# Kernel tuning notes

Hardware: AMD Instinct MI355X
Metric: run time of the kernel (lower is better)

## Reference

```python
import jax, jax.numpy as jnp
import numpy as np
from jax import lax

T, B, E = 512, 128, 128  # timesteps, batch, embedding_size
S = 2 * T                # stack capacity: 2 pushes per step


def setup_inputs() -> dict:
    key = jax.random.key(0)
    k1, k2, k3, k4, k5 = jax.random.split(key, 5)
    return {
        "v1": jax.random.normal(k1, (T, B, E), dtype=jnp.float32),
        "v2": jax.random.normal(k2, (T, B, E), dtype=jnp.float32),
        "d1": jax.random.uniform(k3, (T, B, 1), dtype=jnp.float32),
        "d2": jax.random.uniform(k4, (T, B, 1), dtype=jnp.float32),
        "u": jax.random.uniform(k5, (T, B, 1), dtype=jnp.float32),
    }


def _step(carry, xs):
    strengths, values = carry  # [B,S], [B,S,E]; slots 0..2(t+1)-1 valid after push
    v1t, v2t, d1t, d2t, ut, t = xs  # v*: [B,E]; d*,u: [B,1]; t: scalar int
    # --- push: append two entries at the top (slots 2t, 2t+1) ---
    values = lax.dynamic_update_slice(
        values, jnp.stack([v1t, v2t], axis=1), (0, 2 * t, 0))
    strengths = lax.dynamic_update_slice(
        strengths, jnp.concatenate([d1t, d2t], axis=1), (0, 2 * t))
    # exclusive reverse cumsum = strength used above each slot (top-down order)
    rev_incl = jnp.flip(jnp.cumsum(jnp.flip(strengths, 1), axis=1), 1)  # [B,S]
    used = rev_incl - strengths  # [B,S]
    # --- read: faithful to torch.max(u - strength_used) reducing over batch ---
    m = jnp.max(ut - used, axis=0)            # [S] scalar-over-batch per slot
    w = jnp.minimum(strengths, m[None, :])    # [B,S]; invalid slots hit v=0
    summary = jnp.einsum('bs,bse->be', w, values)  # [B,E]
    # --- pop: s -= min(s, relu(u - used)) using pre-pop strengths ---
    pop_amt = jnp.minimum(strengths, jnp.maximum(0.0, ut - used))
    strengths = strengths - pop_amt
    return (strengths, values), summary


def reference(v1, v2, d1, d2, u):
    init = (jnp.zeros((B, S), v1.dtype), jnp.zeros((B, S, E), v1.dtype))
    ts = jnp.arange(T, dtype=jnp.int32)
    _, out = lax.scan(_step, init, (v1, v2, d1, d2, u, ts))
    return out  # [T,B,E]: read content at each timestep
```

## Files before the change

kernel.cpp:

```cpp
#include <hip/hip_runtime.h>
#include <cstdint>
#include <cstddef>

#define TT 512
#define BB 128
#define EE 128
#define SS 1024
#define NEG_INF (-1e30f)

typedef _Float16 half8 __attribute__((ext_vector_type(8)));
typedef float floatx4 __attribute__((ext_vector_type(4)));

__device__ __forceinline__ unsigned int pkh(float x, float y) {
    _Float16 hx = (_Float16)x, hy = (_Float16)y;
    unsigned short bx, by;
    __builtin_memcpy(&bx, &hx, 2); __builtin_memcpy(&by, &hy, 2);
    return (unsigned int)bx | ((unsigned int)by << 16);
}

__global__ __launch_bounds__(64) void prefixF(
    const float* __restrict__ d1, const float* __restrict__ d2,
    const float* __restrict__ u,
    float* __restrict__ F, float* __restrict__ Bv,
    float* __restrict__ d2T, float* __restrict__ FT,
    float* __restrict__ BvT, float* __restrict__ CST,
    float* __restrict__ CMT, float* __restrict__ HT)
{
    const int b = blockIdx.x;
    const int lane = threadIdx.x;
    const int t0 = lane * 8;

    float l1[8], l2[8], g[8];
#pragma unroll
    for (int j = 0; j < 8; ++j) {
        const int t = t0 + j;
        l1[j] = d1[t * BB + b];
        l2[j] = d2[t * BB + b];
        g[j] = u[t * BB + b] - l1[j] - l2[j];
    }
    float p[8], s = 0.f;
#pragma unroll
    for (int j = 0; j < 8; ++j) { s += g[j]; p[j] = s; }

    float v = s;
#pragma unroll
    for (int off = 1; off < 64; off <<= 1) {
        float o = __shfl_up(v, off);
        if (lane >= off) v += o;
    }
    const float excl = v - s;

    float Fv[8];
#pragma unroll
    for (int j = 0; j < 8; ++j) Fv[j] = excl + p[j];

#pragma unroll
    for (int j = 0; j < 8; ++j) {
        const int t = t0 + j;
        const float Fm1 = (j > 0) ? Fv[j - 1] : excl;
        const float Bvv = Fm1 - l1[j];
        F  [b * TT + t] = Fv[j];
        Bv [b * TT + t] = Bvv;
        d2T[b * TT + t] = l2[j];
        FT [t * BB + b] = Fv[j];
        BvT[t * BB + b] = Bvv;
    }

    float pm[8], sm[8];
    pm[0] = Fv[0];
#pragma unroll
    for (int j = 1; j < 8; ++j) pm[j] = fmaxf(pm[j - 1], Fv[j]);
    sm[7] = Fv[7];
#pragma unroll
    for (int j = 6; j >= 0; --j) sm[j] = fmaxf(sm[j + 1], Fv[j]);

    float pcar = NEG_INF, scar = NEG_INF;
#pragma unroll
    for (int off = 1; off <= 3; ++off) {
        float xu = __shfl_up(pm[7], off);
        if ((lane & 3) >= off) pcar = fmaxf(pcar, xu);
        float xd = __shfl_down(sm[0], off);
        if ((lane & 3) + off <= 3) scar = fmaxf(scar, xd);
    }

#pragma unroll
    for (int j = 0; j < 8; ++j) {
        const int t = t0 + j;
        const float Hv  = fmaxf(pcar, (j > 0) ? pm[j - 1] : NEG_INF);
        const float CSv = fmaxf(sm[j], scar);
        HT [t * BB + b] = Hv;
        CST[t * BB + b] = CSv;
    }
    if ((lane & 3) == 0)
        CMT[(lane >> 2) * BB + b] = fmaxf(sm[0], scar);
}

__global__ __launch_bounds__(256) void calcM2(
    const float* __restrict__ FT, const float* __restrict__ BvT,
    const float* __restrict__ CST, const float* __restrict__ CMT,
    const float* __restrict__ HT, const float* __restrict__ u,
    float* __restrict__ m)
{
    const int t = (int)blockIdx.y;
    const int ci = (int)blockIdx.x;
    const int ct = t >> 5;
    if (ci > ct) return;

    const int tid = threadIdx.x;
    const int b = tid & 127, h = tid >> 7;
    const int ib = 32 * ci;

    __shared__ float cand[BB][66];
    __shared__ float Tot[2][BB];
    __shared__ float red[4][64];

    const float Ft = FT[t * BB + b];

    if (ci < ct) {
        float K = HT[t * BB + b];
        for (int c = ci + 1; c < ct; ++c) K = fmaxf(K, CMT[c * BB + b]);
#pragma unroll
        for (int j = 0; j < 16; ++j) {
            const int jj = 16 * h + j;
            const int i = ib + jj;
            const float R = fmaxf(CST[i * BB + b], K);
            const float Bvv = BvT[i * BB + b];
            cand[b][2 * jj]     = Ft - fmaxf(Bvv, R);
            cand[b][2 * jj + 1] = Ft - R;
        }
    } else {
        float vv[16], sfx[16];
#pragma unroll
        for (int j = 0; j < 16; ++j) {
            const int i = ib + 16 * h + j;
            vv[j] = (i < t) ? FT[i * BB + b] : NEG_INF;
        }
        sfx[15] = vv[15];
#pragma unroll
        for (int j = 14; j >= 0; --j) sfx[j] = fmaxf(vv[j], sfx[j + 1]);
        Tot[h][b] = sfx[0];
        __syncthreads();
        const float carry = (h == 0) ? Tot[1][b] : NEG_INF;
        const float ub = u[t * BB + b];
#pragma unroll
        for (int j = 0; j < 16; ++j) {
            const int jj = 16 * h + j;
            const int i = ib + jj;
            const float R = fmaxf(sfx[j], carry);
            const float Bvv = BvT[i * BB + b];
            cand[b][2 * jj]     = Ft - fmaxf(Bvv, R);
            cand[b][2 * jj + 1] = (i == t) ? ub : (Ft - R);
        }
    }
    __syncthreads();

    {
        const int s = tid & 63, g = tid >> 6;
        float mx = NEG_INF;
        const int b0 = g * 32;
#pragma unroll 8
        for (int bb = b0; bb < b0 + 32; ++bb) mx = fmaxf(mx, cand[bb][s]);
        red[g][s] = mx;
    }
    __syncthreads();
    if (tid < 64) {
        const float r = fmaxf(fmaxf(red[0][tid], red[1][tid]),
                              fmaxf(red[2][tid], red[3][tid]));
        const int s_glob = 64 * ci + tid;
        if (s_glob < 2 * t + 2) m[(size_t)t * SS + s_glob] = r;
    }
}

#define PWH 72
#define PWW 36
#define VTO 2304
#define FRO 6912
#define S0O 7488
#define BVO 8064
#define D2O 8576
#define TPO 8640

__global__ __launch_bounds__(256) void phaseC_mfma(
    const float* __restrict__ F, const float* __restrict__ Bvg,
    const float* __restrict__ d2T, const float* __restrict__ m,
    const float* __restrict__ v1, const float* __restrict__ v2,
    float* __restrict__ out)
{
    const int b  = blockIdx.x & (BB - 1);
    const int wk = blockIdx.x >> 7;

    int tt, ck0, nck;
    if (wk < 6) {
        nck = 8;
        ck0 = (wk == 1) ? 8 : 0;
        tt  = (wk <= 1) ? 7 : 8 - wk;
    } else {
        const int j = wk - 6;
        nck = 6 - 2 * (j >> 1);
        if (j & 1) { tt = 2 - (j >> 1); ck0 = 0; }
        else       { tt = 6 - (j >> 1); ck0 = 8; }
    }
    const int t0 = tt * 64;
    const int ckEnd = ck0 + nck;
    const bool splitTile = (tt >= 4);

    const int tid = threadIdx.x;

    __shared__ float sh[8704];

    const int lane = tid & 63, w = tid >> 6;
    const int wr = w >> 1, wc = w & 1;
    const int n = lane & 15;
    const int kq = (lane >> 4) * 8;
    const int il = tid & 31, g = tid >> 5;
    const int veb = tid & 7;
    const int vip = ((tid >> 3) & 7) + 8 * wc;
    const int veh = wr * 64;

    float4 pv[8];
    float2 pmv[8];

    auto prefetch = [&](int ck) {
        const int ib = 32 * ck;
        const int i = ib + il;
#pragma unroll
        for (int r8 = 0; r8 < 8; ++r8) {
            const int t = t0 + 8 * g + r8;
            pmv[r8] = *(const float2*)&m[(size_t)t * SS + 2 * i];
        }
        const int i0 = ib + 2 * vip, i1 = i0 + 1;
        const float* p10 = v1 + ((size_t)i0 * BB + b) * EE;
        const float* p11 = v1 + ((size_t)i1 * BB + b) * EE;
        const float* p20 = v2 + ((size_t)i0 * BB + b) * EE;
        const float* p21 = v2 + ((size_t)i1 * BB + b) * EE;
#pragma unroll
        for (int c = 0; c < 2; ++c) {
            const int e0 = 4 * veb + 32 * c + veh;
            pv[4 * c + 0] = *(const float4*)&p10[e0];
            pv[4 * c + 1] = *(const float4*)&p11[e0];
            pv[4 * c + 2] = *(const float4*)&p20[e0];
            pv[4 * c + 3] = *(const float4*)&p21[e0];
        }
    };

    const int nF = t0 + 64;
    for (int k = tid; k < nF; k += 256) {
        sh[FRO + k] = F[b * TT + k];
        sh[BVO + k] = Bvg[b * TT + k];
    }
    if (tid < 64) sh[D2O + tid] = d2T[b * TT + t0 + tid];

    prefetch(ck0);

    __syncthreads();

    {
        const int k1 = tid, k2 = tid + 256, k3 = tid + 512;
        sh[S0O + k1] = (k1 < t0) ? sh[FRO + k1] : NEG_INF;
        sh[S0O + k2] = (k2 < t0) ? sh[FRO + k2] : NEG_INF;
        if (k3 < 576) sh[S0O + k3] = NEG_INF;
        if (tid < 64) {
            float xi = sh[FRO + t0 + tid];
#pragma unroll
            for (int off = 1; off < 64; off <<= 1) {
                const float y = __shfl_up(xi, off);
                if (tid >= off) xi = fmaxf(xi, y);
            }
            const float ex = __shfl_up(xi, 1);
            sh[TPO + tid] = (tid == 0) ? NEG_INF : ex;
        }
        __syncthreads();
        for (int off = 1; off < t0; off <<= 1) {
            float a1 = sh[S0O + k1]; if (k1 + off < 576) a1 = fmaxf(a1, sh[S0O + k1 + off]);
            float a2 = sh[S0O + k2]; if (k2 + off < 576) a2 = fmaxf(a2, sh[S0O + k2 + off]);
            __syncthreads();
            sh[S0O + k1] = a1; sh[S0O + k2] = a2;
            __syncthreads();
        }
    }

    float Freg2[8];
#pragma unroll
    for (int j = 0; j < 8; ++j) Freg2[j] = sh[FRO + t0 + 8 * g + j];
    const float qstart = sh[TPO + 8 * g];

    floatx4 acc[2][4];
#pragma unroll
    for (int r = 0; r < 2; ++r)
#pragma unroll
        for (int j = 0; j < 4; ++j) acc[r][j] = (floatx4)0.f;

    for (int ck = ck0; ck < ckEnd; ++ck) {
        const int ib = 32 * ck;
        const int i = ib + il;
        const bool below = (ib < t0);

        unsigned int wreg[8];
        {
            const float Ai = (i > 0) ? sh[FRO + i - 1] : 0.f;
            const float Bi = sh[BVO + i];
            const int li = i - t0;
            float q, S0i = 0.f;
            if (below) {
                S0i = sh[S0O + i];
                q = qstart;
            } else {
                q = NEG_INF;
                for (int k = li; k < 8 * g; ++k)
                    q = fmaxf(q, sh[FRO + t0 + k]);
            }
#pragma unroll
            for (int r8 = 0; r8 < 8; ++r8) {
                const int t_l = 8 * g + r8;
                const float2 mv = pmv[r8];
                float w0 = 0.f, w1 = 0.f;
                if (below) {
                    const float R = fmaxf(S0i, q);
                    const float a0 = fmaxf(Ai, R) - fmaxf(Bi, R);
                    const float a1 = fmaxf(Bi - R, 0.f);
                    w0 = fminf(a0, mv.x);
                    w1 = fminf(a1, mv.y);
                    q = fmaxf(q, Freg2[r8]);
                } else {
                    if (li <= t_l) {
                        const float R = q;
                        const float a0 = fmaxf(Ai, R) - fmaxf(Bi, R);
                        const float a1 = (li == t_l) ? sh[D2O + t_l]
                                                     : fmaxf(Bi - R, 0.f);
                        w0 = fminf(a0, mv.x);
                        w1 = fminf(a1, mv.y);
                    }
                    q = fmaxf(q, (t_l >= li) ? Freg2[r8] : NEG_INF);
                }
                wreg[r8] = pkh(w0, w1);
            }
        }

        uint2 vreg[8];
#pragma unroll
        for (int c = 0; c < 2; ++c) {
            const float4 xa = pv[4 * c + 0], xb = pv[4 * c + 1];
            const float4 ya = pv[4 * c + 2], yb = pv[4 * c + 3];
            vreg[4 * c + 0] = make_uint2(pkh(xa.x, ya.x), pkh(xb.x, yb.x));
            vreg[4 * c + 1] = make_uint2(pkh(xa.y, ya.y), pkh(xb.y, yb.y));
            vreg[4 * c + 2] = make_uint2(pkh(xa.z, ya.z), pkh(xb.z, yb.z));
            vreg[4 * c + 3] = make_uint2(pkh(xa.w, ya.w), pkh(xb.w, yb.w));
        }

        __syncthreads();

#pragma unroll
        for (int r8 = 0; r8 < 8; ++r8)
            ((unsigned int*)sh)[(8 * g + r8) * PWW + il] = wreg[r8];
        {
            unsigned int* vt = (unsigned int*)sh + VTO;
            const int dw = 2 * vip;
#pragma unroll
            for (int c = 0; c < 2; ++c) {
                const int e0 = 4 * veb + 32 * c + veh;
                *(uint2*)&vt[(e0 + 0) * PWW + dw] = vreg[4 * c + 0];
                *(uint2*)&vt[(e0 + 1) * PWW + dw] = vreg[4 * c + 1];
                *(uint2*)&vt[(e0 + 2) * PWW + dw] = vreg[4 * c + 2];
                *(uint2*)&vt[(e0 + 3) * PWW + dw] = vreg[4 * c + 3];
            }
        }

        __syncthreads();

        if (ck + 1 < ckEnd) prefetch(ck + 1);

        __builtin_amdgcn_s_setprio(1);
        {
            const _Float16* WsH = (const _Float16*)sh;
            const _Float16* VtH = (const _Float16*)(sh + VTO);
#pragma unroll
            for (int k2 = 0; k2 < 64; k2 += 32) {
                const half8 av0 = *(const half8*)&WsH[(32 * wr + n) * PWH + kq + k2];
                const half8 av1 = *(const half8*)&WsH[(32 * wr + 16 + n) * PWH + kq + k2];
#pragma unroll
                for (int j = 0; j < 4; ++j) {
                    const half8 bv = *(const half8*)&VtH[(64 * wc + 16 * j + n) * PWH + kq + k2];
                    acc[0][j] = __builtin_amdgcn_mfma_f32_16x16x32_f16(av0, bv, acc[0][j], 0, 0, 0);
                    acc[1][j] = __builtin_amdgcn_mfma_f32_16x16x32_f16(av1, bv, acc[1][j], 0, 0, 0);
                }
            }
        }
        __builtin_amdgcn_s_setprio(0);
    }

    {
        const int q = lane >> 4;
#pragma unroll
        for (int r = 0; r < 2; ++r) {
#pragma unroll
            for (int j = 0; j < 4; ++j) {
#pragma unroll
                for (int reg = 0; reg < 4; ++reg) {
                    const int t = t0 + 32 * wr + 16 * r + 4 * q + reg;
                    const int col = 64 * wc + 16 * j + n;
                    float* dst = &out[((size_t)t * BB + b) * EE + col];
                    if (splitTile) atomicAdd(dst, acc[r][j][reg]);
                    else           *dst = acc[r][j][reg];
                }
            }
        }
    }
}

extern "C" void kernel_launch(void* const* d_in, const int* in_sizes, int n_in,
                              void* d_out, int out_size, void* d_ws, size_t ws_size,
                              hipStream_t stream) {
    const float* v1 = (const float*)d_in[0];
    const float* v2 = (const float*)d_in[1];
    const float* d1 = (const float*)d_in[2];
    const float* d2 = (const float*)d_in[3];
    const float* u  = (const float*)d_in[4];
    float* out = (float*)d_out;

    char* ws = (char*)d_ws;
    float* m   = (float*)ws;
    float* F   = m   + (size_t)TT * SS;
    float* Bvp = F   + (size_t)BB * TT;
    float* d2T = Bvp + (size_t)BB * TT;
    float* FT  = d2T + (size_t)BB * TT;
    float* BvT = FT  + (size_t)BB * TT;
    float* CST = BvT + (size_t)BB * TT;
    float* HT  = CST + (size_t)BB * TT;
    float* CMT = HT  + (size_t)BB * TT;

    hipMemsetAsync(out + (size_t)256 * BB * EE, 0,
                   (size_t)256 * BB * EE * sizeof(float), stream);

    prefixF<<<dim3(BB), dim3(64), 0, stream>>>(d1, d2, u, F, Bvp, d2T, FT,
                                               BvT, CST, CMT, HT);
    calcM2 <<<dim3(16, TT), dim3(256), 0, stream>>>(FT, BvT, CST, CMT, HT, u, m);
    phaseC_mfma<<<dim3(12 * BB), dim3(256), 0, stream>>>(F, Bvp, d2T, m, v1, v2, out);
}
```

Baseline: 207.9 us.

## Replace in-block suffix-max scan with precomputed chunk suffix maxima from prefix kernel

The prefix kernel now also writes a batch-major copy of the per-slot suffix maxima, and the main MFMA kernel combines it with a small 16-entry scan over chunk maxima instead of running a log-step shared-memory suffix-max scan with many barriers over up to 576 entries. Per-slot F, Bv and auxiliary values are prefetched into registers along with the next chunk rather than staged in shared memory, which shrinks LDS use. Launch bounds now request 5 blocks per SM. This trades barrier-heavy setup work for extra global loads and a higher register-pressure constraint.

```diff
diff --git a/kernel.cpp b/kernel.cpp
--- a/kernel.cpp
+++ b/kernel.cpp
@@ -24,7 +24,8 @@
     float* __restrict__ F, float* __restrict__ Bv,
     float* __restrict__ d2T, float* __restrict__ FT,
     float* __restrict__ BvT, float* __restrict__ CST,
-    float* __restrict__ CMT, float* __restrict__ HT)
+    float* __restrict__ CMT, float* __restrict__ HT,
+    float* __restrict__ CSb)
 {
     const int b = blockIdx.x;
     const int lane = threadIdx.x;
@@ -90,6 +91,7 @@
         const float CSv = fmaxf(sm[j], scar);
         HT [t * BB + b] = Hv;
         CST[t * BB + b] = CSv;
+        CSb[b * TT + t] = CSv;
     }
     if ((lane & 3) == 0)
         CMT[(lane >> 2) * BB + b] = fmaxf(sm[0], scar);
@@ -174,15 +176,14 @@
 #define PWH 72
 #define PWW 36
 #define VTO 2304
-#define FRO 6912
-#define S0O 7488
-#define BVO 8064
-#define D2O 8576
-#define TPO 8640
-
-__global__ __launch_bounds__(256) void phaseC_mfma(
+#define TPO 6912
+#define FT0O 6976
+#define SCMO 7040
+
+__global__ __launch_bounds__(256, 5) void phaseC_mfma(
     const float* __restrict__ F, const float* __restrict__ Bvg,
-    const float* __restrict__ d2T, const float* __restrict__ m,
+    const float* __restrict__ d2T, const float* __restrict__ CSb,
+    const float* __restrict__ CMT, const float* __restrict__ m,
     const float* __restrict__ v1, const float* __restrict__ v2,
     float* __restrict__ out)
 {
@@ -201,12 +202,13 @@
         else       { tt = 6 - (j >> 1); ck0 = 8; }
     }
     const int t0 = tt * 64;
+    const int t0c = t0 >> 5;
     const int ckEnd = ck0 + nck;
     const bool splitTile = (tt >= 4);
 
     const int tid = threadIdx.x;
 
-    __shared__ float sh[8704];
+    __shared__ float sh[7056];
 
     const int lane = tid & 63, w = tid >> 6;
     const int wr = w >> 1, wc = w & 1;
@@ -219,16 +221,19 @@
 
     float4 pv[8];
     float2 pmv[8];
+    float pAi, pBi, pAux;
 
     auto prefetch = [&](int ck) {
-        const int ib = 32 * ck;
-        const int i = ib + il;
+        const int i = 32 * ck + il;
 #pragma unroll
         for (int r8 = 0; r8 < 8; ++r8) {
             const int t = t0 + 8 * g + r8;
             pmv[r8] = *(const float2*)&m[(size_t)t * SS + 2 * i];
         }
-        const int i0 = ib + 2 * vip, i1 = i0 + 1;
+        pAi  = F  [b * TT + ((i > 0) ? i - 1 : 0)];
+        pBi  = Bvg[b * TT + i];
+        pAux = (32 * ck < t0) ? CSb[b * TT + i] : d2T[b * TT + i];
+        const int i0 = 32 * ck + 2 * vip, i1 = i0 + 1;
         const float* p10 = v1 + ((size_t)i0 * BB + b) * EE;
         const float* p11 = v1 + ((size_t)i1 * BB + b) * EE;
         const float* p20 = v2 + ((size_t)i0 * BB + b) * EE;
@@ -243,45 +248,35 @@
         }
     };
 
-    const int nF = t0 + 64;
-    for (int k = tid; k < nF; k += 256) {
-        sh[FRO + k] = F[b * TT + k];
-        sh[BVO + k] = Bvg[b * TT + k];
-    }
-    if (tid < 64) sh[D2O + tid] = d2T[b * TT + t0 + tid];
+    if (tid < 64) {
+        float xi = F[b * TT + t0 + tid];
+        sh[FT0O + tid] = xi;
+        float sc = xi;
+#pragma unroll
+        for (int off = 1; off < 64; off <<= 1) {
+            const float y = __shfl_up(sc, off);
+            if (tid >= off) sc = fmaxf(sc, y);
+        }
+        const float ex = __shfl_up(sc, 1);
+        sh[TPO + tid] = (tid == 0) ? NEG_INF : ex;
+    } else if (tid < 128) {
+        const int c = tid - 64;
+        float cm = (c < t0c) ? CMT[c * BB + b] : NEG_INF;
+#pragma unroll
+        for (int off = 1; off < 16; off <<= 1) {
+            const float y = __shfl_down(cm, off);
+            cm = fmaxf(cm, (c + off < 16) ? y : NEG_INF);
+        }
+        if (c < 16) sh[SCMO + c] = cm;
+    }
 
     prefetch(ck0);
 
     __syncthreads();
 
-    {
-        const int k1 = tid, k2 = tid + 256, k3 = tid + 512;
-        sh[S0O + k1] = (k1 < t0) ? sh[FRO + k1] : NEG_INF;
-        sh[S0O + k2] = (k2 < t0) ? sh[FRO + k2] : NEG_INF;
-        if (k3 < 576) sh[S0O + k3] = NEG_INF;
-        if (tid < 64) {
-            float xi = sh[FRO + t0 + tid];
-#pragma unroll
-            for (int off = 1; off < 64; off <<= 1) {
-                const float y = __shfl_up(xi, off);
-                if (tid >= off) xi = fmaxf(xi, y);
-            }
-            const float ex = __shfl_up(xi, 1);
-            sh[TPO + tid] = (tid == 0) ? NEG_INF : ex;
-        }
-        __syncthreads();
-        for (int off = 1; off < t0; off <<= 1) {
-            float a1 = sh[S0O + k1]; if (k1 + off < 576) a1 = fmaxf(a1, sh[S0O + k1 + off]);
-            float a2 = sh[S0O + k2]; if (k2 + off < 576) a2 = fmaxf(a2, sh[S0O + k2 + off]);
-            __syncthreads();
-            sh[S0O + k1] = a1; sh[S0O + k2] = a2;
-            __syncthreads();
-        }
-    }
-
     float Freg2[8];
 #pragma unroll
-    for (int j = 0; j < 8; ++j) Freg2[j] = sh[FRO + t0 + 8 * g + j];
+    for (int j = 0; j < 8; ++j) Freg2[j] = sh[FT0O + 8 * g + j];
     const float qstart = sh[TPO + 8 * g];
 
     floatx4 acc[2][4];
@@ -295,19 +290,30 @@
         const int i = ib + il;
         const bool below = (ib < t0);
 
+        uint2 vreg[8];
+#pragma unroll
+        for (int c = 0; c < 2; ++c) {
+            const float4 xa = pv[4 * c + 0], xb = pv[4 * c + 1];
+            const float4 ya = pv[4 * c + 2], yb = pv[4 * c + 3];
+            vreg[4 * c + 0] = make_uint2(pkh(xa.x, ya.x), pkh(xb.x, yb.x));
+            vreg[4 * c + 1] = make_uint2(pkh(xa.y, ya.y), pkh(xb.y, yb.y));
+            vreg[4 * c + 2] = make_uint2(pkh(xa.z, ya.z), pkh(xb.z, yb.z));
+            vreg[4 * c + 3] = make_uint2(pkh(xa.w, ya.w), pkh(xb.w, yb.w));
+        }
+
         unsigned int wreg[8];
         {
-            const float Ai = (i > 0) ? sh[FRO + i - 1] : 0.f;
-            const float Bi = sh[BVO + i];
+            const float Ai = (i > 0) ? pAi : 0.f;
+            const float Bi = pBi;
             const int li = i - t0;
             float q, S0i = 0.f;
             if (below) {
-                S0i = sh[S0O + i];
+                S0i = fmaxf(pAux, sh[SCMO + ck + 1]);
                 q = qstart;
             } else {
                 q = NEG_INF;
                 for (int k = li; k < 8 * g; ++k)
-                    q = fmaxf(q, sh[FRO + t0 + k]);
+                    q = fmaxf(q, sh[FT0O + k]);
             }
 #pragma unroll
             for (int r8 = 0; r8 < 8; ++r8) {
@@ -325,7 +331,7 @@
                     if (li <= t_l) {
                         const float R = q;
                         const float a0 = fmaxf(Ai, R) - fmaxf(Bi, R);
-                        const float a1 = (li == t_l) ? sh[D2O + t_l]
+                        const float a1 = (li == t_l) ? pAux
                                                      : fmaxf(Bi - R, 0.f);
                         w0 = fminf(a0, mv.x);
                         w1 = fminf(a1, mv.y);
@@ -334,17 +340,6 @@
                 }
                 wreg[r8] = pkh(w0, w1);
             }
-        }
-
-        uint2 vreg[8];
-#pragma unroll
-        for (int c = 0; c < 2; ++c) {
-            const float4 xa = pv[4 * c + 0], xb = pv[4 * c + 1];
-            const float4 ya = pv[4 * c + 2], yb = pv[4 * c + 3];
-            vreg[4 * c + 0] = make_uint2(pkh(xa.x, ya.x), pkh(xb.x, yb.x));
-            vreg[4 * c + 1] = make_uint2(pkh(xa.y, ya.y), pkh(xb.y, yb.y));
-            vreg[4 * c + 2] = make_uint2(pkh(xa.z, ya.z), pkh(xb.z, yb.z));
-            vreg[4 * c + 3] = make_uint2(pkh(xa.w, ya.w), pkh(xb.w, yb.w));
         }
 
         __syncthreads();
@@ -427,12 +422,14 @@
     float* CST = BvT + (size_t)BB * TT;
     float* HT  = CST + (size_t)BB * TT;
     float* CMT = HT  + (size_t)BB * TT;
+    float* CSb = CMT + (size_t)16 * BB;
 
     hipMemsetAsync(out + (size_t)256 * BB * EE, 0,
                    (size_t)256 * BB * EE * sizeof(float), stream);
 
     prefixF<<<dim3(BB), dim3(64), 0, stream>>>(d1, d2, u, F, Bvp, d2T, FT,
-                                               BvT, CST, CMT, HT);
+                                               BvT, CST, CMT, HT, CSb);
     calcM2 <<<dim3(16, TT), dim3(256), 0, stream>>>(FT, BvT, CST, CMT, HT, u, m);
-    phaseC_mfma<<<dim3(12 * BB), dim3(256), 0, stream>>>(F, Bvp, d2T, m, v1, v2, out);
+    phaseC_mfma<<<dim3(12 * BB), dim3(256), 0, stream>>>(F, Bvp, d2T, CSb, CMT,
+                                                         m, v1, v2, out);
 }
```

New measurement: 384.1 us. 84.7% more time.
